# Performance work log

Hardware: AMD Instinct MI355X
Metric: run time of the kernel (lower is better)

Reference implementation:

```python
import jax, jax.numpy as jnp
import numpy as np

V, B, H, NH = 3, 8192, 2048, 16
HD = H // NH
EPS = 1e-5


def setup_inputs() -> dict:
    key = jax.random.key(0)
    ks = jax.random.split(key, 20)
    s = 0.02
    d = {
        "views": jax.random.normal(ks[0], (V, B, H), jnp.float32),
        # per-view query/key/value projections (torch Linear: y = x @ W.T + b)
        "Wq": jax.random.normal(ks[1], (V, H, H)) * s, "bq": jnp.zeros((V, H)),
        "Wk": jax.random.normal(ks[2], (V, H, H)) * s, "bk": jnp.zeros((V, H)),
        "Wv": jax.random.normal(ks[3], (V, H, H)) * s, "bv": jnp.zeros((V, H)),
        # per-view MultiheadAttention internal in_proj (split into q/k/v) and out_proj
        "Wiq": jax.random.normal(ks[4], (V, H, H)) * s, "biq": jnp.zeros((V, H)),
        "Wik": jax.random.normal(ks[5], (V, H, H)) * s, "bik": jnp.zeros((V, H)),
        "Wiv": jax.random.normal(ks[6], (V, H, H)) * s, "biv": jnp.zeros((V, H)),
        "Wo": jax.random.normal(ks[7], (V, H, H)) * s, "bo": jnp.zeros((V, H)),
        # fusion output linear over concatenated views
        "Wout": jax.random.normal(ks[8], (H, V * H)) * s, "bout": jnp.zeros((H,)),
        # LayerNorm
        "gamma": jnp.ones((H,)), "beta": jnp.zeros((H,)),
    }
    return d


def reference(views, Wq, bq, Wk, bk, Wv, bv, Wiq, biq, Wik, bik, Wiv, biv,
              Wo, bo, Wout, bout, gamma, beta):
    # views: [V, B, H]
    # per-view q/k/v projections applied to each view's own embedding
    q = jnp.einsum('vbh,vgh->vbg', views, Wq) + bq[:, None]      # [V,B,H]
    k_all = jnp.einsum('vbh,vgh->vbg', views, Wk) + bk[:, None]  # [V,B,H]
    v_all = jnp.einsum('vbh,vgh->vbg', views, Wv) + bv[:, None]  # [V,B,H]

    # for query view i, keys/values come from all other views (static gather)
    others = jnp.asarray(np.array([[j for j in range(V) if j != i] for i in range(V)]))
    K = k_all[others]   # [V, V-1, B, H]
    Vv = v_all[others]  # [V, V-1, B, H]

    # MultiheadAttention internal in-projections (per query-view i)
    q2 = jnp.einsum('vbh,vgh->vbg', q, Wiq) + biq[:, None]                # [V,B,H]
    k2 = jnp.einsum('vjbh,vgh->vjbg', K, Wik) + bik[:, None, None]        # [V,V-1,B,H]
    v2 = jnp.einsum('vjbh,vgh->vjbg', Vv, Wiv) + biv[:, None, None]       # [V,V-1,B,H]

    qh = q2.reshape(V, B, NH, HD)           # q_len = 1 (squeezed)
    kh = k2.reshape(V, V - 1, B, NH, HD)
    vh = v2.reshape(V, V - 1, B, NH, HD)

    scores = jnp.einsum('vbnd,vjbnd->vbnj', qh, kh) / jnp.sqrt(jnp.float32(HD))
    attn = jax.nn.softmax(scores, axis=-1)  # over the V-1 key views
    ctx = jnp.einsum('vbnj,vjbnd->vbnd', attn, vh).reshape(V, B, H)
    att_out = jnp.einsum('vbh,vgh->vbg', ctx, Wo) + bo[:, None]           # [V,B,H]

    # concat attended outputs per-sample: [B, V*H]
    fused = att_out.transpose(1, 0, 2).reshape(B, V * H)
    projected = fused @ Wout.T + bout

    # residual with first view + LayerNorm (dropout inactive / eval)
    x = views[0] + projected
    mu = jnp.mean(x, axis=-1, keepdims=True)
    var = jnp.mean(jnp.square(x - mu), axis=-1, keepdims=True)
    out = (x - mu) * jax.lax.rsqrt(var + EPS) * gamma + beta
    return out
```

## Files before the change

### kernel.cpp

```cpp
#include <hip/hip_runtime.h>
#include <hip/hip_bf16.h>

typedef __attribute__((ext_vector_type(8))) __bf16 bf16x8;
typedef __attribute__((ext_vector_type(4))) float f32x4;
typedef __hip_bfloat16 bf16_t;

#define BB 8192L
#define HH 2048L
#define BH (8192L*2048L)
#define WUNIT (2048L*2048L)
#define WT (3L*2048L*2048L)
#define LDS_TOTAL 163840

struct SlabMap { int a[6]; int w[6]; };
struct Ptrs4 { const float* in[4]; bf16_t* out[4]; };
struct FoldJob { const float* W2; const float* b1; const float* badd; float* out; int ld; };
struct FoldPack { FoldJob j[16]; };
struct GJob { const bf16_t* A; const bf16_t* Bw; bf16_t* C; int lda; int ldc; };
struct GJobs { GJob j[18]; };

__device__ __forceinline__ void gload_lds16(const void* g, void* l) {
    __builtin_amdgcn_global_load_lds((__attribute__((address_space(1))) void*)g,
                                     (__attribute__((address_space(3))) void*)l, 16, 0, 0);
}

template<bool OUT_F32, bool FUSEK>
__device__ __forceinline__ void gemm_core(
    const bf16_t* __restrict__ A, int lda, long aslab,
    const bf16_t* __restrict__ Wb, int ldb,
    const float* __restrict__ be,
    void* __restrict__ Cout, int ldc,
    long rowA0, long rowB0, int K, char* lds)
{
    const int tid  = threadIdx.x;
    const int lane = tid & 63;
    const int w    = tid >> 6;
    const int wm   = w >> 2, wn = w & 3;

    const int srow    = tid >> 3;
    const int schunk8 = ((tid & 7) ^ (srow & 7)) * 8;
    const int wuni    = w * 1024;
    const int NK = K >> 6;

    auto stageA = [&](int s) {
        char* dst = lds + (s % 3) * 32768;
        const int k0 = s << 6;
        const bf16_t* Aeff; int ka;
        if constexpr (FUSEK) { Aeff = A + (long)(k0 >> 11) * aslab; ka = k0 & 2047; }
        else                 { Aeff = A; ka = k0; }
        #pragma unroll
        for (int i = 0; i < 4; ++i)
            gload_lds16(Aeff + (rowA0 + i*64 + srow) * (long)lda + (ka + schunk8), dst + i*8192 + wuni);
    };
    auto stageB = [&](int s, int q) {
        char* dst = lds + 98304 + (s & 1) * 32768 + q*16384;
        const int k0 = s << 6;
        #pragma unroll
        for (int j = 0; j < 2; ++j)
            gload_lds16(Wb + (rowB0 + q*128 + j*64 + srow) * (long)ldb + (k0 + schunk8), dst + j*8192 + wuni);
    };

    f32x4 acc[8][4];
    const f32x4 zero = {0.f, 0.f, 0.f, 0.f};
    #pragma unroll
    for (int i = 0; i < 8; ++i)
        #pragma unroll
        for (int j = 0; j < 4; ++j) acc[i][j] = zero;

    stageA(0); stageB(0,0); stageB(0,1);
    stageA(1); stageB(1,0); stageB(1,1);
    asm volatile("s_waitcnt vmcnt(8)" ::: "memory");
    asm volatile("s_barrier" ::: "memory");

    const int arow16 = wm*128 + (lane & 15);
    const int brow16 = wn*64  + (lane & 15);
    const int kb     = (lane >> 4) * 16;

    #define LDSA(row, kh) (*(const bf16x8*)(bufA + (row)*128 + (((kh)*64 + kb) ^ (((row) & 7) << 4))))
    #define LDSB(row, kh) (*(const bf16x8*)(bufB + (row)*128 + (((kh)*64 + kb) ^ (((row) & 7) << 4))))

    for (int s = 0; s < NK; ++s) {
        char* bufA = lds + (s % 3) * 32768;
        char* bufB = lds + 98304 + (s & 1) * 32768;
        bf16x8 a[4][2], b0[2][2], b1[2][2];

        if (s + 2 < NK) stageA(s + 2);
        #pragma unroll
        for (int cf = 0; cf < 2; ++cf) {
            const int r = brow16 + cf*16;
            #pragma unroll
            for (int kh = 0; kh < 2; ++kh) b0[cf][kh] = LDSB(r, kh);
        }
        #pragma unroll
        for (int rf = 0; rf < 4; ++rf) {
            const int r = arow16 + rf*16;
            #pragma unroll
            for (int kh = 0; kh < 2; ++kh) a[rf][kh] = LDSA(r, kh);
        }
        asm volatile("s_barrier" ::: "memory");
        __builtin_amdgcn_sched_barrier(0);
        __builtin_amdgcn_s_setprio(1);
        #pragma unroll
        for (int kh = 0; kh < 2; ++kh)
            #pragma unroll
            for (int rf = 0; rf < 4; ++rf)
                #pragma unroll
                for (int cf = 0; cf < 2; ++cf)
                    acc[rf][cf] = __builtin_amdgcn_mfma_f32_16x16x32_bf16(a[rf][kh], b0[cf][kh], acc[rf][cf], 0, 0, 0);
        __builtin_amdgcn_s_setprio(0);

        #pragma unroll
        for (int cf = 0; cf < 2; ++cf) {
            const int r = brow16 + 32 + cf*16;
            #pragma unroll
            for (int kh = 0; kh < 2; ++kh) b1[cf][kh] = LDSB(r, kh);
        }
        asm volatile("s_barrier" ::: "memory");
        __builtin_amdgcn_sched_barrier(0);
        __builtin_amdgcn_s_setprio(1);
        #pragma unroll
        for (int kh = 0; kh < 2; ++kh)
            #pragma unroll
            for (int rf = 0; rf < 4; ++rf)
                #pragma unroll
                for (int cf = 0; cf < 2; ++cf)
                    acc[rf][2+cf] = __builtin_amdgcn_mfma_f32_16x16x32_bf16(a[rf][kh], b1[cf][kh], acc[rf][2+cf], 0, 0, 0);
        __builtin_amdgcn_s_setprio(0);

        if (s + 2 < NK) stageB(s + 2, 0);
        #pragma unroll
        for (int rf = 0; rf < 4; ++rf) {
            const int r = arow16 + 64 + rf*16;
            #pragma unroll
            for (int kh = 0; kh < 2; ++kh) a[rf][kh] = LDSA(r, kh);
        }
        asm volatile("s_barrier" ::: "memory");
        __builtin_amdgcn_sched_barrier(0);
        __builtin_amdgcn_s_setprio(1);
        #pragma unroll
        for (int kh = 0; kh < 2; ++kh)
            #pragma unroll
            for (int rf = 0; rf < 4; ++rf)
                #pragma unroll
                for (int cf = 0; cf < 2; ++cf)
                    acc[4+rf][cf] = __builtin_amdgcn_mfma_f32_16x16x32_bf16(a[rf][kh], b0[cf][kh], acc[4+rf][cf], 0, 0, 0);
        __builtin_amdgcn_s_setprio(0);

        if (s + 2 < NK) stageB(s + 2, 1);
        if (s + 1 < NK) {
            if (s + 2 < NK) asm volatile("s_waitcnt vmcnt(8)" ::: "memory");
            else            asm volatile("s_waitcnt vmcnt(0)" ::: "memory");
            asm volatile("s_barrier" ::: "memory");
            __builtin_amdgcn_sched_barrier(0);
        }
        __builtin_amdgcn_s_setprio(1);
        #pragma unroll
        for (int kh = 0; kh < 2; ++kh)
            #pragma unroll
            for (int rf = 0; rf < 4; ++rf)
                #pragma unroll
                for (int cf = 0; cf < 2; ++cf)
                    acc[4+rf][2+cf] = __builtin_amdgcn_mfma_f32_16x16x32_bf16(a[rf][kh], b1[cf][kh], acc[4+rf][2+cf], 0, 0, 0);
        __builtin_amdgcn_s_setprio(0);
    }
    #undef LDSA
    #undef LDSB

    const long crow0 = rowA0 + wm*128 + ((lane >> 4) * 4);
    const int  ccol0 = (int)rowB0 + wn*64 + (lane & 15);
    #pragma unroll
    for (int rf = 0; rf < 8; ++rf) {
        #pragma unroll
        for (int cf = 0; cf < 4; ++cf) {
            const int col = ccol0 + cf*16;
            const float bv = be ? be[col] : 0.f;
            #pragma unroll
            for (int r = 0; r < 4; ++r) {
                const long row = crow0 + rf*16 + r;
                const float val = acc[rf][cf][r] + bv;
                if constexpr (OUT_F32) ((float*)Cout)[row*(long)ldc + col] = val;
                else ((bf16_t*)Cout)[row*(long)ldc + col] = __float2bfloat16(val);
            }
        }
    }
}

template<bool OUT_F32, bool FUSEK>
__global__ __launch_bounds__(512, 1)
void gemm256(const bf16_t* __restrict__ A, int lda, long aslab, SlabMap map, int mshift,
             const bf16_t* __restrict__ Bw, int ldb,
             const float* __restrict__ bias,
             void* __restrict__ Cout, int ldc, long cslab, int K)
{
    extern __shared__ char lds[];
    const int nwg = (int)gridDim.x;
    const int wid = (int)blockIdx.x;
    const int swz = (wid & 7) * (nwg >> 3) + (wid >> 3);
    const int bx  = swz & 7;
    const int by  = swz >> 3;

    const int  sl    = by >> mshift;
    const long rowA0 = (long)(by & ((1 << mshift) - 1)) * 256;
    const long rowB0 = (long)bx * 256;
    const bf16_t* Ab = FUSEK ? A : (A + (long)map.a[sl] * aslab);
    const bf16_t* Wb = Bw + (long)map.w[sl] * WUNIT;
    const float*  be = bias ? (bias + (long)map.w[sl] * HH) : nullptr;
    const long cbase = (long)sl * cslab;
    void* Cj = OUT_F32 ? (void*)((float*)Cout + cbase) : (void*)((bf16_t*)Cout + cbase);
    gemm_core<OUT_F32, FUSEK>(Ab, lda, aslab, Wb, ldb, be, Cj, ldc, rowA0, rowB0, K, lds);
}

__global__ __launch_bounds__(512, 1)
void gemm_fold(GJobs js)
{
    extern __shared__ char lds[];
    const int nwg = (int)gridDim.x;
    const int wid = (int)blockIdx.x;
    const int swz = (wid & 7) * (nwg >> 3) + (wid >> 3);
    const GJob jb = js.j[swz >> 6];
    const int inner = swz & 63;
    const long rowA0 = (long)(inner >> 3) * 256;
    const long rowB0 = (long)(inner & 7) * 256;
    gemm_core<false, false>(jb.A, jb.lda, 0L, jb.Bw, 2048, nullptr,
                            (void*)jb.C, jb.ldc, rowA0, rowB0, 2048, lds);
}

__global__ __launch_bounds__(256)
void f2b_kernel(const float* __restrict__ in, bf16_t* __restrict__ out, long n)
{
    long i = ((long)blockIdx.x * 256 + threadIdx.x) * 4;
    const long stride = (long)gridDim.x * 256 * 4;
    for (; i < n; i += stride) {
        const float4 v = *(const float4*)(in + i);
        __hip_bfloat162 lo, hi;
        lo.x = __float2bfloat16(v.x); lo.y = __float2bfloat16(v.y);
        hi.x = __float2bfloat16(v.z); hi.y = __float2bfloat16(v.w);
        *(__hip_bfloat162*)(out + i)     = lo;
        *(__hip_bfloat162*)(out + i + 2) = hi;
    }
}

__global__ __launch_bounds__(256)
void f2b4_kernel(Ptrs4 p)
{
    const long total = 4 * WT;
    long i = ((long)blockIdx.x * 256 + threadIdx.x) * 4;
    const long stride = (long)gridDim.x * 256 * 4;
    for (; i < total; i += stride) {
        const int  t   = (int)(i / WT);
        const long off = i - (long)t * WT;
        const float4 v = *(const float4*)(p.in[t] + off);
        __hip_bfloat162 lo, hi;
        lo.x = __float2bfloat16(v.x); lo.y = __float2bfloat16(v.y);
        hi.x = __float2bfloat16(v.z); hi.y = __float2bfloat16(v.w);
        *(__hip_bfloat162*)(p.out[t] + off)     = lo;
        *(__hip_bfloat162*)(p.out[t] + off + 2) = hi;
    }
}

__global__ __launch_bounds__(256)
void f2bT4_kernel(Ptrs4 p)
{
    __shared__ float sm[64][65];
    const int gmat = blockIdx.x >> 10;
    const int t    = gmat / 3, m = gmat % 3;
    const int tile = blockIdx.x & 1023;
    const int tr   = tile >> 5, tc = tile & 31;
    const int lr = threadIdx.x >> 4;
    const int lc = (threadIdx.x & 15) * 4;
    const float* src = p.in[t] + (long)m*WUNIT + ((long)tr*64)*2048 + tc*64;
    #pragma unroll
    for (int it = 0; it < 4; ++it) {
        const int r = lr + it*16;
        const float4 v = *(const float4*)(src + (long)r*2048 + lc);
        sm[r][lc] = v.x; sm[r][lc+1] = v.y; sm[r][lc+2] = v.z; sm[r][lc+3] = v.w;
    }
    __syncthreads();
    bf16_t* dst = p.out[t] + (long)m*WUNIT + ((long)tc*64)*2048 + tr*64;
    #pragma unroll
    for (int it = 0; it < 4; ++it) {
        const int r = lr + it*16;
        __hip_bfloat162 p0, p1;
        p0.x = __float2bfloat16(sm[lc+0][r]); p0.y = __float2bfloat16(sm[lc+1][r]);
        p1.x = __float2bfloat16(sm[lc+2][r]); p1.y = __float2bfloat16(sm[lc+3][r]);
        *(__hip_bfloat162*)(dst + (long)r*2048 + lc)     = p0;
        *(__hip_bfloat162*)(dst + (long)r*2048 + lc + 2) = p1;
    }
}

__global__ __launch_bounds__(256)
void biasfold_all(FoldPack p)
{
    const FoldJob jb = p.j[blockIdx.x >> 11];
    const int g2 = blockIdx.x & 2047;
    const int t  = threadIdx.x;
    float s = 0.f;
    for (int k = t; k < jb.ld; k += 256) s += jb.W2[(long)g2*jb.ld + k] * jb.b1[k];
    #pragma unroll
    for (int off = 32; off > 0; off >>= 1) s += __shfl_xor(s, off);
    __shared__ float rs[4];
    if ((t & 63) == 0) rs[t >> 6] = s;
    __syncthreads();
    if (t == 0) jb.out[g2] = rs[0] + rs[1] + rs[2] + rs[3] + jb.badd[g2];
}

__global__ __launch_bounds__(256)
void attn_kernel(const bf16_t* __restrict__ q2, const bf16_t* __restrict__ k2,
                 const bf16_t* __restrict__ v2, bf16_t* __restrict__ ctx, int bshift)
{
    const long gw = (long)blockIdx.x * 4 + (threadIdx.x >> 6);
    const int lane = threadIdx.x & 63;
    const int  v_  = (int)(gw >> (bshift + 4));
    const long rem = gw & ((1L << (bshift + 4)) - 1);
    const long b   = rem >> 4;
    const int  n   = (int)(rem & 15);
    const long base = ((((long)v_ << bshift) + b)) * HH + (long)n * 128 + lane * 2;

    const __hip_bfloat162 qv = *(const __hip_bfloat162*)(q2 + base);
    const float q0 = __bfloat162float(qv.x), q1 = __bfloat162float(qv.y);
    float s[2], va[2], vb[2];
    #pragma unroll
    for (int j = 0; j < 2; ++j) {
        const long kb = ((((long)(v_*2 + j) << bshift) + b)) * HH + (long)n * 128 + lane * 2;
        const __hip_bfloat162 kv = *(const __hip_bfloat162*)(k2 + kb);
        float p = q0 * __bfloat162float(kv.x) + q1 * __bfloat162float(kv.y);
        #pragma unroll
        for (int off = 32; off > 0; off >>= 1) p += __shfl_xor(p, off);
        s[j] = p;
        const __hip_bfloat162 vv = *(const __hip_bfloat162*)(v2 + kb);
        va[j] = __bfloat162float(vv.x); vb[j] = __bfloat162float(vv.y);
    }
    const float scale = 0.08838834764831845f;
    const float s0 = s[0] * scale, s1 = s[1] * scale;
    const float m  = fmaxf(s0, s1);
    const float e0 = expf(s0 - m), e1 = expf(s1 - m);
    const float inv = 1.0f / (e0 + e1);
    const float a0 = e0 * inv, a1 = e1 * inv;
    __hip_bfloat162 o;
    o.x = __float2bfloat16(a0 * va[0] + a1 * va[1]);
    o.y = __float2bfloat16(a0 * vb[0] + a1 * vb[1]);
    *(__hip_bfloat162*)(ctx + base) = o;
}

__global__ __launch_bounds__(256)
void ln_kernel(const float* __restrict__ proj, const float* __restrict__ v0,
               const float* __restrict__ gamma, const float* __restrict__ beta,
               float* __restrict__ out)
{
    const long b = blockIdx.x;
    const int t = threadIdx.x;
    const float* pr = proj + b * HH;
    const float* vw = v0 + b * HH;
    float x[8]; float s = 0.f, s2 = 0.f;
    #pragma unroll
    for (int k = 0; k < 8; ++k) {
        const int idx = t + k * 256;
        x[k] = vw[idx] + pr[idx];
        s += x[k]; s2 += x[k] * x[k];
    }
    #pragma unroll
    for (int off = 32; off > 0; off >>= 1) { s += __shfl_xor(s, off); s2 += __shfl_xor(s2, off); }
    __shared__ float rs[4], rs2[4];
    if ((t & 63) == 0) { rs[t >> 6] = s; rs2[t >> 6] = s2; }
    __syncthreads();
    s  = rs[0] + rs[1] + rs[2] + rs[3];
    s2 = rs2[0] + rs2[1] + rs2[2] + rs2[3];
    const float mu  = s * (1.0f / 2048.0f);
    const float var = s2 * (1.0f / 2048.0f) - mu * mu;
    const float rstd = rsqrtf(var + 1e-5f);
    #pragma unroll
    for (int k = 0; k < 8; ++k) {
        const int idx = t + k * 256;
        out[b * HH + idx] = (x[k] - mu) * rstd * gamma[idx] + beta[idx];
    }
}

extern "C" void kernel_launch(void* const* d_in, const int* in_sizes, int n_in,
                              void* d_out, int out_size, void* d_ws, size_t ws_size,
                              hipStream_t stream)
{
    const float* views = (const float*)d_in[0];
    const float* Wq   = (const float*)d_in[1];  const float* bq   = (const float*)d_in[2];
    const float* Wk   = (const float*)d_in[3];  const float* bk   = (const float*)d_in[4];
    const float* Wv   = (const float*)d_in[5];  const float* bv   = (const float*)d_in[6];
    const float* Wiq  = (const float*)d_in[7];  const float* biq  = (const float*)d_in[8];
    const float* Wik  = (const float*)d_in[9];  const float* bik  = (const float*)d_in[10];
    const float* Wiv  = (const float*)d_in[11]; const float* biv  = (const float*)d_in[12];
    const float* Wo   = (const float*)d_in[13]; const float* bo   = (const float*)d_in[14];
    const float* Wout = (const float*)d_in[15]; const float* bout = (const float*)d_in[16];
    const float* gamma= (const float*)d_in[17]; const float* beta = (const float*)d_in[18];

    static bool attr_set = false;
    if (!attr_set) {
        hipFuncSetAttribute((const void*)gemm256<false,false>,
                            hipFuncAttributeMaxDynamicSharedMemorySize, LDS_TOTAL);
        hipFuncSetAttribute((const void*)gemm256<true,true>,
                            hipFuncAttributeMaxDynamicSharedMemorySize, LDS_TOTAL);
        hipFuncSetAttribute((const void*)gemm_fold,
                            hipFuncAttributeMaxDynamicSharedMemorySize, LDS_TOTAL);
        attr_set = true;
    }

    char* ws = (char*)d_ws;
    bf16_t* WQ2  = (bf16_t*)ws;
    bf16_t* WK2  = WQ2 + 3*WUNIT;
    bf16_t* WV2  = WK2 + 6*WUNIT;
    bf16_t* WFIN = WV2 + 6*WUNIT;
    float*  BQ2  = (float*)(WFIN + 3*WUNIT);
    float*  BK2  = BQ2 + 3*HH;
    float*  BV2  = BK2 + 6*HH;
    float*  BFIN = BV2 + 6*HH;
    const long FIXED = 18L*WUNIT*2 + 16L*HH*4;

    char* R = ws + FIXED;
    bf16_t* WIQ   = (bf16_t*)R;
    bf16_t* WIK   = WIQ  + 3*WUNIT;
    bf16_t* WIV   = WIK  + 3*WUNIT;
    bf16_t* WOUTB = WIV  + 3*WUNIT;
    bf16_t* WQT   = WOUTB+ 3*WUNIT;
    bf16_t* WKT   = WQT  + 3*WUNIT;
    bf16_t* WVT   = WKT  + 3*WUNIT;
    bf16_t* WOT   = WVT  + 3*WUNIT;

    const long scratch = 24L*WUNIT*2;
    long Bc = 8192;
    while (Bc > 256) {
        long need = Bc * 73728L; if (need < scratch) need = scratch;
        if (FIXED + need <= (long)ws_size) break;
        Bc >>= 1;
    }
    const int mshift = __builtin_ctzl((unsigned long)Bc) - 8;
    const int bshift = __builtin_ctzl((unsigned long)Bc);
    const long S1 = Bc * HH;

    bf16_t* VBF = (bf16_t*)R;
    bf16_t* Q2B = VBF + 3*S1;
    bf16_t* K2  = Q2B + 3*S1;
    bf16_t* V2  = K2  + 6*S1;
    float*  PROJ= (float*)K2;

    const SlabMap mp3  = {{0,1,2,0,0,0},{0,1,2,0,0,0}};
    const SlabMap mp6k = {{1,2,0,2,0,1},{0,1,2,3,4,5}};
    const SlabMap mp1  = {{0,0,0,0,0,0},{0,0,0,0,0,0}};
    const int oth[3][2] = {{1,2},{0,2},{0,1}};

    {
        Ptrs4 c1 = {{Wiq, Wik, Wiv, Wout}, {WIQ, WIK, WIV, WOUTB}};
        f2b4_kernel<<<8192, 256, 0, stream>>>(c1);
        Ptrs4 c2 = {{Wq, Wk, Wv, Wo}, {WQT, WKT, WVT, WOT}};
        f2bT4_kernel<<<12288, 256, 0, stream>>>(c2);
    }
    {
        GJobs js;
        for (int v = 0; v < 3; ++v)
            js.j[v] = { WIQ + (long)v*WUNIT, WQT + (long)v*WUNIT, WQ2 + (long)v*WUNIT, 2048, 2048 };
        for (int v = 0; v < 3; ++v)
            for (int j = 0; j < 2; ++j) {
                const int p = v*2 + j, o = oth[v][j];
                js.j[3 + p] = { WIK + (long)v*WUNIT, WKT + (long)o*WUNIT, WK2 + (long)p*WUNIT, 2048, 2048 };
                js.j[9 + p] = { WIV + (long)v*WUNIT, WVT + (long)o*WUNIT, WV2 + (long)p*WUNIT, 2048, 2048 };
            }
        for (int v = 0; v < 3; ++v)
            js.j[15 + v] = { WOUTB + (long)v*2048, WOT + (long)v*WUNIT, WFIN + (long)v*2048, 6144, 6144 };
        gemm_fold<<<1152, 512, LDS_TOTAL, stream>>>(js);
    }
    {
        FoldPack fp;
        for (int v = 0; v < 3; ++v)
            fp.j[v] = { Wiq + (long)v*WUNIT, bq + v*HH, biq + v*HH, BQ2 + v*HH, 2048 };
        for (int v = 0; v < 3; ++v)
            for (int j = 0; j < 2; ++j) {
                const int p = v*2 + j, o = oth[v][j];
                fp.j[3 + p] = { Wik + (long)v*WUNIT, bk + o*HH, bik + v*HH, BK2 + p*HH, 2048 };
                fp.j[9 + p] = { Wiv + (long)v*WUNIT, bv + o*HH, biv + v*HH, BV2 + p*HH, 2048 };
            }
        fp.j[15] = { Wout, bo, bout, BFIN, 6144 };
        biasfold_all<<<32768, 256, 0, stream>>>(fp);
    }

    const int nwg3 = 8 * 3 * (int)(Bc >> 8);
    const int nwg6 = 8 * 6 * (int)(Bc >> 8);
    const int nwg1 = 8 * 1 * (int)(Bc >> 8);
    const int vgrid = (int)((S1 / 1024 > 8192) ? 8192 : S1 / 1024);

    for (long b0 = 0; b0 < BB; b0 += Bc) {
        if (Bc == 8192) {
            f2b_kernel<<<8192, 256, 0, stream>>>(views, VBF, 3*BH);
        } else {
            for (int v = 0; v < 3; ++v)
                f2b_kernel<<<vgrid, 256, 0, stream>>>(views + v*BH + b0*HH, VBF + v*S1, S1);
        }
        gemm256<false,false><<<nwg3, 512, LDS_TOTAL, stream>>>(VBF, 2048, S1, mp3,  mshift, WQ2, 2048, BQ2, (void*)Q2B, 2048, S1, 2048);
        gemm256<false,false><<<nwg6, 512, LDS_TOTAL, stream>>>(VBF, 2048, S1, mp6k, mshift, WK2, 2048, BK2, (void*)K2,  2048, S1, 2048);
        gemm256<false,false><<<nwg6, 512, LDS_TOTAL, stream>>>(VBF, 2048, S1, mp6k, mshift, WV2, 2048, BV2, (void*)V2,  2048, S1, 2048);
        attn_kernel<<<(int)(12*Bc), 256, 0, stream>>>(Q2B, K2, V2, VBF, bshift);
        gemm256<true,true><<<nwg1, 512, LDS_TOTAL, stream>>>(VBF, 2048, S1, mp1, mshift, WFIN, 6144, BFIN, (void*)PROJ, 2048, 0, 6144);
        ln_kernel<<<(int)Bc, 256, 0, stream>>>(PROJ, views + b0*HH, gamma, beta, ((float*)d_out) + b0*HH);
    }
}
```

Before: 1.647 ms.

## Simplify GEMM main loop to double-buffered B with fewer barriers

```diff
diff --git a/kernel.cpp b/kernel.cpp
--- a/kernel.cpp
+++ b/kernel.cpp
@@ -52,12 +52,12 @@
         for (int i = 0; i < 4; ++i)
             gload_lds16(Aeff + (rowA0 + i*64 + srow) * (long)lda + (ka + schunk8), dst + i*8192 + wuni);
     };
-    auto stageB = [&](int s, int q) {
-        char* dst = lds + 98304 + (s & 1) * 32768 + q*16384;
+    auto stageB = [&](int s) {
+        char* dst = lds + 98304 + (s & 1) * 32768;
         const int k0 = s << 6;
         #pragma unroll
-        for (int j = 0; j < 2; ++j)
-            gload_lds16(Wb + (rowB0 + q*128 + j*64 + srow) * (long)ldb + (k0 + schunk8), dst + j*8192 + wuni);
+        for (int i = 0; i < 4; ++i)
+            gload_lds16(Wb + (rowB0 + i*64 + srow) * (long)ldb + (k0 + schunk8), dst + i*8192 + wuni);
     };
 
     f32x4 acc[8][4];
@@ -67,9 +67,8 @@
         #pragma unroll
         for (int j = 0; j < 4; ++j) acc[i][j] = zero;
 
-    stageA(0); stageB(0,0); stageB(0,1);
-    stageA(1); stageB(1,0); stageB(1,1);
-    asm volatile("s_waitcnt vmcnt(8)" ::: "memory");
+    stageA(0); stageB(0); stageA(1);
+    asm volatile("s_waitcnt vmcnt(4)" ::: "memory");
     asm volatile("s_barrier" ::: "memory");
 
     const int arow16 = wm*128 + (lane & 15);
@@ -84,12 +83,16 @@
         char* bufB = lds + 98304 + (s & 1) * 32768;
         bf16x8 a[4][2], b0[2][2], b1[2][2];
 
+        if (s + 1 < NK) stageB(s + 1);
         if (s + 2 < NK) stageA(s + 2);
+
         #pragma unroll
         for (int cf = 0; cf < 2; ++cf) {
-            const int r = brow16 + cf*16;
-            #pragma unroll
-            for (int kh = 0; kh < 2; ++kh) b0[cf][kh] = LDSB(r, kh);
+            #pragma unroll
+            for (int kh = 0; kh < 2; ++kh) {
+                b0[cf][kh] = LDSB(brow16 + cf*16, kh);
+                b1[cf][kh] = LDSB(brow16 + 32 + cf*16, kh);
+            }
         }
         #pragma unroll
         for (int rf = 0; rf < 4; ++rf) {
@@ -97,71 +100,37 @@
             #pragma unroll
             for (int kh = 0; kh < 2; ++kh) a[rf][kh] = LDSA(r, kh);
         }
-        asm volatile("s_barrier" ::: "memory");
-        __builtin_amdgcn_sched_barrier(0);
-        __builtin_amdgcn_s_setprio(1);
         #pragma unroll
         for (int kh = 0; kh < 2; ++kh)
             #pragma unroll
             for (int rf = 0; rf < 4; ++rf)
                 #pragma unroll
-                for (int cf = 0; cf < 2; ++cf)
-                    acc[rf][cf] = __builtin_amdgcn_mfma_f32_16x16x32_bf16(a[rf][kh], b0[cf][kh], acc[rf][cf], 0, 0, 0);
-        __builtin_amdgcn_s_setprio(0);
-
-        #pragma unroll
-        for (int cf = 0; cf < 2; ++cf) {
-            const int r = brow16 + 32 + cf*16;
-            #pragma unroll
-            for (int kh = 0; kh < 2; ++kh) b1[cf][kh] = LDSB(r, kh);
-        }
-        asm volatile("s_barrier" ::: "memory");
-        __builtin_amdgcn_sched_barrier(0);
-        __builtin_amdgcn_s_setprio(1);
+                for (int cf = 0; cf < 2; ++cf) {
+                    acc[rf][cf]   = __builtin_amdgcn_mfma_f32_16x16x32_bf16(a[rf][kh], b0[cf][kh], acc[rf][cf],   0, 0, 0);
+                    acc[rf][2+cf] = __builtin_amdgcn_mfma_f32_16x16x32_bf16(a[rf][kh], b1[cf][kh], acc[rf][2+cf], 0, 0, 0);
+                }
+
+        #pragma unroll
+        for (int rf = 0; rf < 4; ++rf) {
+            const int r = arow16 + 64 + rf*16;
+            #pragma unroll
+            for (int kh = 0; kh < 2; ++kh) a[rf][kh] = LDSA(r, kh);
+        }
         #pragma unroll
         for (int kh = 0; kh < 2; ++kh)
             #pragma unroll
             for (int rf = 0; rf < 4; ++rf)
                 #pragma unroll
-                for (int cf = 0; cf < 2; ++cf)
-                    acc[rf][2+cf] = __builtin_amdgcn_mfma_f32_16x16x32_bf16(a[rf][kh], b1[cf][kh], acc[rf][2+cf], 0, 0, 0);
-        __builtin_amdgcn_s_setprio(0);
-
-        if (s + 2 < NK) stageB(s + 2, 0);
-        #pragma unroll
-        for (int rf = 0; rf < 4; ++rf) {
-            const int r = arow16 + 64 + rf*16;
-            #pragma unroll
-            for (int kh = 0; kh < 2; ++kh) a[rf][kh] = LDSA(r, kh);
-        }
-        asm volatile("s_barrier" ::: "memory");
-        __builtin_amdgcn_sched_barrier(0);
-        __builtin_amdgcn_s_setprio(1);
-        #pragma unroll
-        for (int kh = 0; kh < 2; ++kh)
-            #pragma unroll
-            for (int rf = 0; rf < 4; ++rf)
-                #pragma unroll
-                for (int cf = 0; cf < 2; ++cf)
-                    acc[4+rf][cf] = __builtin_amdgcn_mfma_f32_16x16x32_bf16(a[rf][kh], b0[cf][kh], acc[4+rf][cf], 0, 0, 0);
-        __builtin_amdgcn_s_setprio(0);
-
-        if (s + 2 < NK) stageB(s + 2, 1);
+                for (int cf = 0; cf < 2; ++cf) {
+                    acc[4+rf][cf]   = __builtin_amdgcn_mfma_f32_16x16x32_bf16(a[rf][kh], b0[cf][kh], acc[4+rf][cf],   0, 0, 0);
+                    acc[4+rf][2+cf] = __builtin_amdgcn_mfma_f32_16x16x32_bf16(a[rf][kh], b1[cf][kh], acc[4+rf][2+cf], 0, 0, 0);
+                }
+
         if (s + 1 < NK) {
-            if (s + 2 < NK) asm volatile("s_waitcnt vmcnt(8)" ::: "memory");
+            if (s + 2 < NK) asm volatile("s_waitcnt vmcnt(4)" ::: "memory");
             else            asm volatile("s_waitcnt vmcnt(0)" ::: "memory");
             asm volatile("s_barrier" ::: "memory");
-            __builtin_amdgcn_sched_barrier(0);
-        }
-        __builtin_amdgcn_s_setprio(1);
-        #pragma unroll
-        for (int kh = 0; kh < 2; ++kh)
-            #pragma unroll
-            for (int rf = 0; rf < 4; ++rf)
-                #pragma unroll
-                for (int cf = 0; cf < 2; ++cf)
-                    acc[4+rf][2+cf] = __builtin_amdgcn_mfma_f32_16x16x32_bf16(a[rf][kh], b1[cf][kh], acc[4+rf][2+cf], 0, 0, 0);
-        __builtin_amdgcn_s_setprio(0);
+        }
     }
     #undef LDSA
     #undef LDSB
@@ -478,9 +447,9 @@
         biasfold_all<<<32768, 256, 0, stream>>>(fp);
     }
 
-    const int nwg3 = 8 * 3 * (int)(Bc >> 8);
-    const int nwg6 = 8 * 6 * (int)(Bc >> 8);
-    const int nwg1 = 8 * 1 * (int)(Bc >> 8);
+    const int nwg3  = 8 * 3 * (int)(Bc >> 8);
+    const int nwg6  = 8 * 6 * (int)(Bc >> 8);
+    const int nwg1  = 8 * 1 * (int)(Bc >> 8);
     const int vgrid = (int)((S1 / 1024 > 8192) ? 8192 : S1 / 1024);
 
     for (long b0 = 0; b0 < BB; b0 += Bc) {
```

After: 1.745 ms. 1.06x slower.
